# Kernel optimization log

Hardware: AMD Instinct MI355X
Metric: run time of the kernel (lower is better)

## Reference

```python
import jax, jax.numpy as jnp
import numpy as np

N, M, D, NNZ, H = 1024, 1024, 128, 32768, 256


def setup_inputs() -> dict:
    key = jax.random.key(0)
    k_x, k_v, k_e, k_w1, k_b1, k_w2, k_b2 = jax.random.split(key, 7)
    X = jax.random.normal(k_x, (N, D), dtype=jnp.float32)
    V = jax.random.randint(k_v, (NNZ,), 0, N)
    E = jax.random.randint(k_e, (NNZ,), 0, M)
    # nn.Linear(2D, 256) and nn.Linear(256, 1) params (Kaiming-uniform-ish init)
    lim1 = 1.0 / np.sqrt(2 * D)
    W1 = jax.random.uniform(k_w1, (2 * D, H), minval=-lim1, maxval=lim1, dtype=jnp.float32)
    b1 = jax.random.uniform(k_b1, (H,), minval=-lim1, maxval=lim1, dtype=jnp.float32)
    lim2 = 1.0 / np.sqrt(H)
    W2 = jax.random.uniform(k_w2, (H, 1), minval=-lim2, maxval=lim2, dtype=jnp.float32)
    b2 = jax.random.uniform(k_b2, (1,), minval=-lim2, maxval=lim2, dtype=jnp.float32)
    return {"X": X, "V": V, "E": E, "W1": W1, "b1": b1, "W2": W2, "b2": b2}


def reference(X, V, E, W1, b1, W2, b2):
    # scatter-mean: eX[m] = mean of X[V[j]] over j with E[j] == m  -> [M, D]
    gathered = X[V]  # [NNZ, D]
    sums = jax.ops.segment_sum(gathered, E, num_segments=M)           # [M, D]
    counts = jax.ops.segment_sum(jnp.ones((NNZ,), X.dtype), E, num_segments=M)
    eX = sums / jnp.maximum(counts, 1.0)[:, None]
    # cat([X_broadcast, eX_broadcast], -1) @ W1 == X @ W1[:D] + eX @ W1[D:]
    # avoids materializing the [N, M, 2D] concat; math is identical.
    hx = X @ W1[:D]    # [N, H]
    he = eX @ W1[D:]   # [M, H]
    h = jax.nn.relu(hx[:, None, :] + he[None, :, :] + b1)  # [N, M, H]
    logits = jnp.squeeze(h @ W2, axis=-1) + b2              # [N, M]
    return jax.nn.sigmoid(logits)
```

## Files before the change

kernel.cpp:

```cpp
#include <hip/hip_runtime.h>

#define N_ 1024
#define M_ 1024
#define D_ 128
#define NNZ_ 32768
#define H_ 256

typedef _Float16 h2 __attribute__((ext_vector_type(2)));

__global__ __launch_bounds__(512) void gemm_kernel(
        const float* __restrict__ X, const int* __restrict__ V,
        const int* __restrict__ E, const float* __restrict__ W1,
        const float* __restrict__ b1,
        _Float16* __restrict__ hx, _Float16* __restrict__ heb) {
    __shared__ float sA[8][128];
    __shared__ int s_bkt[4][128];
    __shared__ int s_cnt[4];
    const int t = threadIdx.x;
    const int b = blockIdx.x;
    const int row0 = b * 4;
    const int m0 = b * 4;
    const int u = t & 255;

    if (t < 128)
        ((float4*)&sA[0][0])[t] = ((const float4*)(X + row0 * D_))[t];
    if (t >= 256 && t < 260) s_cnt[t - 256] = 0;
    __syncthreads();

    float acc[4];
#pragma unroll
    for (int r = 0; r < 4; ++r) acc[r] = 0.f;

    if (t < 256) {
        const float* __restrict__ Wa = W1;
        for (int dd = 0; dd < D_; dd += 4) {
            float w0 = Wa[(dd + 0) * H_ + t];
            float w1 = Wa[(dd + 1) * H_ + t];
            float w2 = Wa[(dd + 2) * H_ + t];
            float w3 = Wa[(dd + 3) * H_ + t];
#pragma unroll
            for (int r = 0; r < 4; ++r) {
                float4 a = *(const float4*)&sA[r][dd];
                acc[r] = fmaf(a.x, w0, acc[r]);
                acc[r] = fmaf(a.y, w1, acc[r]);
                acc[r] = fmaf(a.z, w2, acc[r]);
                acc[r] = fmaf(a.w, w3, acc[r]);
            }
        }
    } else {
        const int4* E4 = (const int4*)E;
        const int4* V4 = (const int4*)V;
#pragma unroll 4
        for (int it = 0; it < NNZ_ / 4 / 256; ++it) {
            int idx = it * 256 + u;
            int4 e4 = E4[idx];
            unsigned r0 = (unsigned)(e4.x - m0);
            unsigned r1 = (unsigned)(e4.y - m0);
            unsigned r2 = (unsigned)(e4.z - m0);
            unsigned r3 = (unsigned)(e4.w - m0);
            if ((r0 < 4u) | (r1 < 4u) | (r2 < 4u) | (r3 < 4u)) {
                int4 v4 = V4[idx];
                if (r0 < 4u) { int s = atomicAdd(&s_cnt[r0], 1); s_bkt[r0][s & 127] = v4.x; }
                if (r1 < 4u) { int s = atomicAdd(&s_cnt[r1], 1); s_bkt[r1][s & 127] = v4.y; }
                if (r2 < 4u) { int s = atomicAdd(&s_cnt[r2], 1); s_bkt[r2][s & 127] = v4.z; }
                if (r3 < 4u) { int s = atomicAdd(&s_cnt[r3], 1); s_bkt[r3][s & 127] = v4.w; }
            }
        }
    }
    __syncthreads();

    if (t < 256) {
#pragma unroll
        for (int r = 0; r < 4; ++r)
            hx[(row0 + r) * H_ + t] = (_Float16)acc[r];
    }
    {
        const int d = t & 127;
        const int r = t >> 7;
        const int cnt = min(s_cnt[r], 128);
        float s = 0.f;
        int i = 0;
        for (; i + 8 <= cnt; i += 8) {
            int v0 = s_bkt[r][i],     v1 = s_bkt[r][i + 1];
            int v2 = s_bkt[r][i + 2], v3 = s_bkt[r][i + 3];
            int v4 = s_bkt[r][i + 4], v5 = s_bkt[r][i + 5];
            int v6 = s_bkt[r][i + 6], v7 = s_bkt[r][i + 7];
            s += X[v0 * D_ + d];
            s += X[v1 * D_ + d];
            s += X[v2 * D_ + d];
            s += X[v3 * D_ + d];
            s += X[v4 * D_ + d];
            s += X[v5 * D_ + d];
            s += X[v6 * D_ + d];
            s += X[v7 * D_ + d];
        }
        for (; i + 4 <= cnt; i += 4) {
            int v0 = s_bkt[r][i],     v1 = s_bkt[r][i + 1];
            int v2 = s_bkt[r][i + 2], v3 = s_bkt[r][i + 3];
            s += X[v0 * D_ + d];
            s += X[v1 * D_ + d];
            s += X[v2 * D_ + d];
            s += X[v3 * D_ + d];
        }
        for (; i < cnt; ++i) s += X[s_bkt[r][i] * D_ + d];
        sA[4 + r][d] = s;
    }
    __syncthreads();

    {
        const int rbase = (t < 256) ? 0 : 2;
        float acc2[2];
        acc2[0] = 0.f;
        acc2[1] = 0.f;
        const float* __restrict__ Wb = W1 + D_ * H_;
        for (int dd = 0; dd < D_; dd += 4) {
            float w0 = Wb[(dd + 0) * H_ + u];
            float w1 = Wb[(dd + 1) * H_ + u];
            float w2 = Wb[(dd + 2) * H_ + u];
            float w3 = Wb[(dd + 3) * H_ + u];
#pragma unroll
            for (int r = 0; r < 2; ++r) {
                float4 a = *(const float4*)&sA[4 + rbase + r][dd];
                acc2[r] = fmaf(a.x, w0, acc2[r]);
                acc2[r] = fmaf(a.y, w1, acc2[r]);
                acc2[r] = fmaf(a.z, w2, acc2[r]);
                acc2[r] = fmaf(a.w, w3, acc2[r]);
            }
        }
        const float bias = b1[u];
#pragma unroll
        for (int r = 0; r < 2; ++r) {
            float inv = 1.0f / fmaxf((float)s_cnt[rbase + r], 1.0f);
            heb[(m0 + rbase + r) * H_ + u] = (_Float16)(acc2[r] * inv + bias);
        }
    }
}

__global__ __launch_bounds__(512) void big_kernel(
        const _Float16* __restrict__ hx, const _Float16* __restrict__ heb,
        const float* __restrict__ W2, const float* __restrict__ b2,
        float* __restrict__ out) {
    __shared__ _Float16 sA[64][264];
    __shared__ _Float16 sB[64][264];
    __shared__ h2 sW[H_ / 2];

    const int tid = threadIdx.x;
    const int tx = tid & 15;
    const int ty = tid >> 4;
    const int n0 = blockIdx.y * 64;
    const int m0 = blockIdx.x * 64;

    if (tid < H_ / 2) {
        h2 w;
        w.x = (_Float16)W2[2 * tid];
        w.y = (_Float16)W2[2 * tid + 1];
        sW[tid] = w;
    }

    {
        const float4* A4 = (const float4*)hx;
        const float4* B4 = (const float4*)heb;
#pragma unroll
        for (int it = 0; it < 4; ++it) {
            int lin = it * 512 + tid;
            int row = lin >> 5;
            int c = lin & 31;
            *(float4*)&sA[row][c * 8] = A4[(n0 + row) * 32 + c];
            *(float4*)&sB[row][c * 8] = B4[(m0 + row) * 32 + c];
        }
    }
    __syncthreads();

    float acc[2][4];
#pragma unroll
    for (int i = 0; i < 2; ++i)
#pragma unroll
        for (int j = 0; j < 4; ++j) acc[i][j] = 0.f;

    union Vn { float4 f4; h2 h[4]; };
    const h2 z = {(_Float16)0.f, (_Float16)0.f};

#pragma unroll 4
    for (int hp = 0; hp < H_ / 2; hp += 4) {
        Vn av[2], bv[4], wv;
        wv.f4 = *(const float4*)&sW[hp];
#pragma unroll
        for (int i = 0; i < 2; ++i) av[i].f4 = *(const float4*)&sA[ty + 32 * i][hp * 2];
#pragma unroll
        for (int j = 0; j < 4; ++j) bv[j].f4 = *(const float4*)&sB[tx + 16 * j][hp * 2];
#pragma unroll
        for (int k = 0; k < 4; ++k) {
#pragma unroll
            for (int i = 0; i < 2; ++i) {
#pragma unroll
                for (int j = 0; j < 4; ++j) {
                    h2 s = av[i].h[k] + bv[j].h[k];
                    s = __builtin_elementwise_max(s, z);
                    acc[i][j] = __builtin_amdgcn_fdot2(s, wv.h[k], acc[i][j], false);
                }
            }
        }
    }

    const float bb = b2[0];
#pragma unroll
    for (int i = 0; i < 2; ++i) {
#pragma unroll
        for (int j = 0; j < 4; ++j) {
            float x = acc[i][j] + bb;
            out[(n0 + ty + 32 * i) * M_ + (m0 + tx + 16 * j)] =
                1.0f / (1.0f + __expf(-x));
        }
    }
}

extern "C" void kernel_launch(void* const* d_in, const int* in_sizes, int n_in,
                              void* d_out, int out_size, void* d_ws, size_t ws_size,
                              hipStream_t stream) {
    const float* X  = (const float*)d_in[0];
    const int*   V  = (const int*)d_in[1];
    const int*   E  = (const int*)d_in[2];
    const float* W1 = (const float*)d_in[3];
    const float* b1 = (const float*)d_in[4];
    const float* W2 = (const float*)d_in[5];
    const float* b2 = (const float*)d_in[6];
    float* out = (float*)d_out;

    char* ws = (char*)d_ws;
    _Float16* hx  = (_Float16*)(ws);
    _Float16* heb = (_Float16*)(ws + 524288);

    gemm_kernel<<<256, 512, 0, stream>>>(X, V, E, W1, b1, hx, heb);

    dim3 bgrid(M_ / 64, N_ / 64);
    big_kernel<<<bgrid, 512, 0, stream>>>(hx, heb, W2, b2, out);
}
```

Baseline: 101.3 us.

## Split big_kernel H loads into two halves to overlap second-half stores with compute

New measurement: 106.3 us. +5.0%, slower.

```diff
diff --git a/kernel.cpp b/kernel.cpp
--- a/kernel.cpp
+++ b/kernel.cpp
@@ -33,6 +33,7 @@
 
     if (t < 256) {
         const float* __restrict__ Wa = W1;
+#pragma unroll 2
         for (int dd = 0; dd < D_; dd += 4) {
             float w0 = Wa[(dd + 0) * H_ + t];
             float w1 = Wa[(dd + 1) * H_ + t];
@@ -50,7 +51,7 @@
     } else {
         const int4* E4 = (const int4*)E;
         const int4* V4 = (const int4*)V;
-#pragma unroll 4
+#pragma unroll 8
         for (int it = 0; it < NNZ_ / 4 / 256; ++it) {
             int idx = it * 256 + u;
             int4 e4 = E4[idx];
@@ -113,6 +114,7 @@
         acc2[0] = 0.f;
         acc2[1] = 0.f;
         const float* __restrict__ Wb = W1 + D_ * H_;
+#pragma unroll 2
         for (int dd = 0; dd < D_; dd += 4) {
             float w0 = Wb[(dd + 0) * H_ + u];
             float w1 = Wb[(dd + 1) * H_ + u];
@@ -140,8 +142,8 @@
         const _Float16* __restrict__ hx, const _Float16* __restrict__ heb,
         const float* __restrict__ W2, const float* __restrict__ b2,
         float* __restrict__ out) {
-    __shared__ _Float16 sA[64][264];
-    __shared__ _Float16 sB[64][264];
+    __shared__ _Float16 sA[2][64][136];
+    __shared__ _Float16 sB[2][64][136];
     __shared__ h2 sW[H_ / 2];
 
     const int tid = threadIdx.x;
@@ -157,17 +159,29 @@
         sW[tid] = w;
     }
 
-    {
-        const float4* A4 = (const float4*)hx;
-        const float4* B4 = (const float4*)heb;
-#pragma unroll
-        for (int it = 0; it < 4; ++it) {
-            int lin = it * 512 + tid;
-            int row = lin >> 5;
-            int c = lin & 31;
-            *(float4*)&sA[row][c * 8] = A4[(n0 + row) * 32 + c];
-            *(float4*)&sB[row][c * 8] = B4[(m0 + row) * 32 + c];
-        }
+    const float4* A4 = (const float4*)hx;
+    const float4* B4 = (const float4*)heb;
+    float4 ra0[2], rb0[2], ra1[2], rb1[2];
+#pragma unroll
+    for (int it = 0; it < 2; ++it) {
+        int lin = it * 512 + tid;
+        int row = lin >> 4, c = lin & 15;
+        ra0[it] = A4[(n0 + row) * 32 + c];
+        rb0[it] = B4[(m0 + row) * 32 + c];
+    }
+#pragma unroll
+    for (int it = 0; it < 2; ++it) {
+        int lin = it * 512 + tid;
+        int row = lin >> 4, c = lin & 15;
+        ra1[it] = A4[(n0 + row) * 32 + 16 + c];
+        rb1[it] = B4[(m0 + row) * 32 + 16 + c];
+    }
+#pragma unroll
+    for (int it = 0; it < 2; ++it) {
+        int lin = it * 512 + tid;
+        int row = lin >> 4, c = lin & 15;
+        *(float4*)&sA[0][row][c * 8] = ra0[it];
+        *(float4*)&sB[0][row][c * 8] = rb0[it];
     }
     __syncthreads();
 
@@ -181,13 +195,44 @@
     const h2 z = {(_Float16)0.f, (_Float16)0.f};
 
 #pragma unroll 4
-    for (int hp = 0; hp < H_ / 2; hp += 4) {
+    for (int hp = 0; hp < 64; hp += 4) {
         Vn av[2], bv[4], wv;
         wv.f4 = *(const float4*)&sW[hp];
 #pragma unroll
-        for (int i = 0; i < 2; ++i) av[i].f4 = *(const float4*)&sA[ty + 32 * i][hp * 2];
-#pragma unroll
-        for (int j = 0; j < 4; ++j) bv[j].f4 = *(const float4*)&sB[tx + 16 * j][hp * 2];
+        for (int i = 0; i < 2; ++i) av[i].f4 = *(const float4*)&sA[0][ty + 32 * i][hp * 2];
+#pragma unroll
+        for (int j = 0; j < 4; ++j) bv[j].f4 = *(const float4*)&sB[0][tx + 16 * j][hp * 2];
+#pragma unroll
+        for (int k = 0; k < 4; ++k) {
+#pragma unroll
+            for (int i = 0; i < 2; ++i) {
+#pragma unroll
+                for (int j = 0; j < 4; ++j) {
+                    h2 s = av[i].h[k] + bv[j].h[k];
+                    s = __builtin_elementwise_max(s, z);
+                    acc[i][j] = __builtin_amdgcn_fdot2(s, wv.h[k], acc[i][j], false);
+                }
+            }
+        }
+    }
+
+#pragma unroll
+    for (int it = 0; it < 2; ++it) {
+        int lin = it * 512 + tid;
+        int row = lin >> 4, c = lin & 15;
+        *(float4*)&sA[1][row][c * 8] = ra1[it];
+        *(float4*)&sB[1][row][c * 8] = rb1[it];
+    }
+    __syncthreads();
+
+#pragma unroll 4
+    for (int hp = 0; hp < 64; hp += 4) {
+        Vn av[2], bv[4], wv;
+        wv.f4 = *(const float4*)&sW[64 + hp];
+#pragma unroll
+        for (int i = 0; i < 2; ++i) av[i].f4 = *(const float4*)&sA[1][ty + 32 * i][hp * 2];
+#pragma unroll
+        for (int j = 0; j < 4; ++j) bv[j].f4 = *(const float4*)&sB[1][tx + 16 * j][hp * 2];
 #pragma unroll
         for (int k = 0; k < 4; ++k) {
 #pragma unroll
```
